# Kernel optimization log

Measured on AMD Instinct MI355X. Metric: run time of the kernel, lower is better.

The kernel has to match this reference:

```python
import jax, jax.numpy as jnp
import numpy as np

D_MODEL = 2048
N_EXPERTS = 64


def setup_inputs() -> dict:
    key = jax.random.key(0)
    kx, kw = jax.random.split(key)
    x = jax.random.normal(kx, (4, 4096, D_MODEL), dtype=jnp.float32)
    # nn.Linear(d_model, n_experts, bias=False): weight [n_experts, d_model]
    W = jax.random.normal(kw, (N_EXPERTS, D_MODEL), dtype=jnp.float32) * (1.0 / np.sqrt(D_MODEL))
    return {"x": x, "W": W, "n_active": 2, "capacity": 4096}


def reference(x, W, n_active, capacity):
    # router_logits = x @ W^T : [b, s, e]
    router_logits = jnp.einsum("bsd,ed->bse", x, W)
    router_probs = jax.nn.softmax(router_logits, axis=-1)
    # top-k over experts
    scores, expert_indices = jax.lax.top_k(router_probs, n_active)  # [b, s, k]
    scores = scores / jnp.sum(scores, axis=-1, keepdims=True)
    n_experts = router_probs.shape[-1]
    # scatter normalized scores into dense gate tensor [b, s, e]
    # (top-k indices are distinct, so one-hot sum == torch scatter_)
    gates = jnp.sum(
        jax.nn.one_hot(expert_indices, n_experts, dtype=scores.dtype) * scores[..., None],
        axis=-2,
    )
    expert_counts = jnp.sum(gates, axis=(0, 1))  # [e]
    load_loss = jnp.mean((expert_counts / jnp.sum(expert_counts) * n_experts - 1.0) ** 2)
    return gates, expert_indices, load_loss
```

## Files before the change

### kernel.cpp

```cpp
#include <hip/hip_runtime.h>
#include <hip/hip_bf16.h>
#include <math.h>

#define TOK_TOTAL 16384
#define D_MODEL   2048
#define NEXP      64
#define BM        32
#define KC        64
#define NCH       (D_MODEL / KC)
#define NBLK      (TOK_TOTAL / BM)
#define TAU       1e-3f

#define IDX_OFF   (TOK_TOTAL * NEXP)
#define LOSS_OFF  (IDX_OFF + TOK_TOTAL * 2)

#define WS_WL     65536
#define WS_CNTP   (2 * 65536)
#define WS_RCNT   (WS_CNTP + NBLK * NEXP)
#define WS_RLIST  (WS_RCNT + 1)

typedef __attribute__((ext_vector_type(8))) short short8_t;
typedef __attribute__((ext_vector_type(4))) float f32x4;

__device__ __forceinline__ short cvh(float f) {
    return __builtin_bit_cast(short, __float2bfloat16(f));
}
__device__ __forceinline__ short cvl(float f) {
    __hip_bfloat16 h = __float2bfloat16(f);
    return __builtin_bit_cast(short, __float2bfloat16(f - __bfloat162float(h)));
}

__device__ __forceinline__ void gload16(const void* gp, void* lp) {
    __builtin_amdgcn_global_load_lds(
        (const __attribute__((address_space(1))) void*)gp,
        (__attribute__((address_space(3))) void*)lp, 16, 0, 0);
}

__global__ __launch_bounds__(256, 1)
void build_wt(const float* __restrict__ W, short8_t* __restrict__ WH8,
              short8_t* __restrict__ WL8, int* __restrict__ rep_cnt)
{
    const int id = blockIdx.x * 256 + threadIdx.x;
    if (id == 0) *rep_cnt = 0;
    const int k8 = id & 255, e = id >> 8;
    float4 a = *(const float4*)(W + (long)e * D_MODEL + k8 * 8);
    float4 b = *(const float4*)(W + (long)e * D_MODEL + k8 * 8 + 4);
    short8_t h8, l8;
    h8[0]=cvh(a.x); h8[1]=cvh(a.y); h8[2]=cvh(a.z); h8[3]=cvh(a.w);
    h8[4]=cvh(b.x); h8[5]=cvh(b.y); h8[6]=cvh(b.z); h8[7]=cvh(b.w);
    l8[0]=cvl(a.x); l8[1]=cvl(a.y); l8[2]=cvl(a.z); l8[3]=cvl(a.w);
    l8[4]=cvl(b.x); l8[5]=cvl(b.y); l8[6]=cvl(b.z); l8[7]=cvl(b.w);
    WH8[k8 * NEXP + e] = h8;
    WL8[k8 * NEXP + e] = l8;
}

__global__ __launch_bounds__(256, 2)
void router_gemm(const float* __restrict__ x,
                 const short8_t* __restrict__ WH8, const short8_t* __restrict__ WL8,
                 float* __restrict__ out, float* __restrict__ cntp,
                 int* __restrict__ rep_cnt, int* __restrict__ rep_list)
{
    __shared__ __align__(16) float    sxf[2][BM][KC];
    __shared__ __align__(16) short8_t swh[2][8][NEXP];
    __shared__ __align__(16) short8_t swl[2][8][NEXP];
    __shared__ float4 s_ig[BM];

    const int t = threadIdx.x;
    const int w = t >> 6, l = t & 63;
    const int tg = w >> 1, eg = w & 1;
    const int lane16 = l & 15, kq = l >> 4;
    const long tok0 = (long)blockIdx.x * BM;
    const int arow = tg * 16 + lane16;

    f32x4 acc0 = (f32x4){0.f,0.f,0.f,0.f};
    f32x4 acc1 = (f32x4){0.f,0.f,0.f,0.f};

    auto STAGE = [&](int c, int buf) {
        #pragma unroll
        for (int j = 0; j < 2; ++j) {
            const int rbase = w * 8 + j * 4;
            const int r  = rbase + (l >> 4);
            const int s4 = (l & 15) ^ (r & 15);
            gload16(x + (tok0 + r) * D_MODEL + c * KC + s4 * 4, &sxf[buf][rbase][0]);
        }
        #pragma unroll
        for (int j = 0; j < 2; ++j) {
            const int k8 = w * 2 + j;
            gload16(WH8 + ((long)c * 8 + k8) * NEXP + l, &swh[buf][k8][0]);
            gload16(WL8 + ((long)c * 8 + k8) * NEXP + l, &swl[buf][k8][0]);
        }
    };

    auto COMPUTE = [&](int buf) {
        #pragma unroll
        for (int seg = 0; seg < 2; ++seg) {
            const int c4  = seg * 8 + kq * 2;
            f32x4 fa = *(const f32x4*)&sxf[buf][arow][((c4    ) ^ lane16) * 4];
            f32x4 fb = *(const f32x4*)&sxf[buf][arow][((c4 + 1) ^ lane16) * 4];
            short8_t ah, al;
            ah[0]=cvh(fa[0]); ah[1]=cvh(fa[1]); ah[2]=cvh(fa[2]); ah[3]=cvh(fa[3]);
            ah[4]=cvh(fb[0]); ah[5]=cvh(fb[1]); ah[6]=cvh(fb[2]); ah[7]=cvh(fb[3]);
            al[0]=cvl(fa[0]); al[1]=cvl(fa[1]); al[2]=cvl(fa[2]); al[3]=cvl(fa[3]);
            al[4]=cvl(fb[0]); al[5]=cvl(fb[1]); al[6]=cvl(fb[2]); al[7]=cvl(fb[3]);
            const int k8 = seg * 4 + kq;
            short8_t bh0 = swh[buf][k8][eg * 32 + lane16];
            short8_t bl0 = swl[buf][k8][eg * 32 + lane16];
            short8_t bh1 = swh[buf][k8][eg * 32 + 16 + lane16];
            short8_t bl1 = swl[buf][k8][eg * 32 + 16 + lane16];
            acc0 = __builtin_amdgcn_mfma_f32_16x16x32_bf16(ah, bl0, acc0, 0, 0, 0);
            acc0 = __builtin_amdgcn_mfma_f32_16x16x32_bf16(al, bh0, acc0, 0, 0, 0);
            acc0 = __builtin_amdgcn_mfma_f32_16x16x32_bf16(ah, bh0, acc0, 0, 0, 0);
            acc1 = __builtin_amdgcn_mfma_f32_16x16x32_bf16(ah, bl1, acc1, 0, 0, 0);
            acc1 = __builtin_amdgcn_mfma_f32_16x16x32_bf16(al, bh1, acc1, 0, 0, 0);
            acc1 = __builtin_amdgcn_mfma_f32_16x16x32_bf16(ah, bh1, acc1, 0, 0, 0);
        }
    };

    STAGE(0, 0);
    __syncthreads();

    for (int c = 0; c < NCH; ++c) {
        const int buf = c & 1;
        if (c + 1 < NCH) STAGE(c + 1, buf ^ 1);
        COMPUTE(buf);
        __syncthreads();
    }

    float* Lg = (float*)&sxf[0][0][0];
    {
        const int trow = tg * 16 + kq * 4;
        #pragma unroll
        for (int r = 0; r < 4; ++r) {
            Lg[(trow + r) * 68 + eg * 32 + lane16]      = acc0[r];
            Lg[(trow + r) * 68 + eg * 32 + 16 + lane16] = acc1[r];
        }
    }
    __syncthreads();

    if (t < BM) {
        const float* lrow = Lg + t * 68;
        float b0 = -1e30f, b1 = -1e30f, b2 = -1e30f;
        int i0 = 0, i1 = 0;
        for (int e = 0; e < NEXP; ++e) {
            float v = lrow[e];
            if (v > b0)      { b2 = b1; b1 = b0; i1 = i0; b0 = v; i0 = e; }
            else if (v > b1) { b2 = b1; b1 = v; i1 = e; }
            else if (v > b2) { b2 = v; }
        }
        float ex = __expf(b1 - b0);
        float g0 = 1.f / (1.f + ex);
        long tok = tok0 + t;
        out[IDX_OFF + 2 * tok]     = (float)i0;
        out[IDX_OFF + 2 * tok + 1] = (float)i1;
        s_ig[t] = make_float4((float)i0, (float)i1, g0, ex * g0);
        if ((b0 - b1 < TAU) || (b1 - b2 < TAU)) {
            int p = atomicAdd(rep_cnt, 1);
            rep_list[p] = (int)tok;
        }
    }
    __syncthreads();

    {
        const int r8 = t >> 3, e0 = (t & 7) * 8;
        float4 gg = s_ig[r8];
        const int i0 = (int)gg.x, i1 = (int)gg.y;
        float v[8];
        #pragma unroll
        for (int j = 0; j < 8; ++j) {
            int e = e0 + j;
            v[j] = (e == i0) ? gg.z : ((e == i1) ? gg.w : 0.f);
        }
        float* orow = out + (tok0 + r8) * NEXP + e0;
        *(float4*)(orow)     = make_float4(v[0], v[1], v[2], v[3]);
        *(float4*)(orow + 4) = make_float4(v[4], v[5], v[6], v[7]);
    }

    if (t < NEXP) {
        float cs = 0.f;
        for (int tt = 0; tt < BM; ++tt) {
            float4 gg = s_ig[tt];
            if ((int)gg.x == t) cs += gg.z;
            if ((int)gg.y == t) cs += gg.w;
        }
        cntp[blockIdx.x * NEXP + t] = cs;
    }
}

__global__ __launch_bounds__(256, 1)
void router_tail(const float* __restrict__ x, const float* __restrict__ W,
                 float* __restrict__ out, const float* __restrict__ cntp,
                 const int* __restrict__ rep_cnt, const int* __restrict__ rep_list)
{
    const int t = threadIdx.x;

    if (blockIdx.x == 0) {
        __shared__ double red[4][NEXP];
        const int e = t & 63, p = t >> 6;
        double s = 0.0;
        for (int b = 0; b < NBLK / 4; ++b)
            s += (double)cntp[(p * (NBLK / 4) + b) * NEXP + e];
        red[p][e] = s;
        __syncthreads();
        if (t == 0) {
            double sc[NEXP], tot = 0.0;
            for (int i = 0; i < NEXP; ++i) {
                sc[i] = red[0][i] + red[1][i] + red[2][i] + red[3][i];
                tot += sc[i];
            }
            double loss = 0.0;
            for (int i = 0; i < NEXP; ++i) {
                double d = sc[i] / tot * (double)NEXP - 1.0;
                loss += d * d;
            }
            out[LOSS_OFF] = (float)(loss / NEXP);
        }
        return;
    }

    __shared__ double red[4][NEXP];
    const int nf = *rep_cnt;
    const int e = t & 63, part = t >> 6;
    for (int i = (int)blockIdx.x - 1; i < nf; i += (int)gridDim.x - 1) {
        const long tok = rep_list[i];
        const float* xr = x + tok * D_MODEL;
        const float* wr = W + (long)e * D_MODEL;
        const int k0 = part * 512;
        double s = 0.0;
        for (int kk = 0; kk < 512; kk += 4) {
            float4 xv = *(const float4*)(xr + k0 + kk);
            float4 wv = *(const float4*)(wr + k0 + kk);
            s = fma((double)xv.x, (double)wv.x, s);
            s = fma((double)xv.y, (double)wv.y, s);
            s = fma((double)xv.z, (double)wv.z, s);
            s = fma((double)xv.w, (double)wv.w, s);
        }
        red[part][e] = s;
        __syncthreads();
        if (t == 0) {
            double best = -1e300, sec = -1e300;
            int bi = 0, si = 0;
            for (int ee = 0; ee < NEXP; ++ee) {
                double vv = red[0][ee] + red[1][ee] + red[2][ee] + red[3][ee];
                if (vv > best)     { sec = best; si = bi; best = vv; bi = ee; }
                else if (vv > sec) { sec = vv; si = ee; }
            }
            out[IDX_OFF + 2 * tok]     = (float)bi;
            out[IDX_OFF + 2 * tok + 1] = (float)si;
        }
        __syncthreads();
    }
}

extern "C" void kernel_launch(void* const* d_in, const int* in_sizes, int n_in,
                              void* d_out, int out_size, void* d_ws, size_t ws_size,
                              hipStream_t stream)
{
    const float* x = (const float*)d_in[0];
    const float* W = (const float*)d_in[1];
    float* out = (float*)d_out;
    float* ws  = (float*)d_ws;
    short8_t* WH8 = (short8_t*)ws;
    short8_t* WL8 = (short8_t*)(ws + WS_WL);
    float* cntp = ws + WS_CNTP;
    int* rep_cnt  = (int*)(ws + WS_RCNT);
    int* rep_list = (int*)(ws + WS_RLIST);

    build_wt   <<<64, 256, 0, stream>>>(W, WH8, WL8, rep_cnt);
    router_gemm<<<NBLK, 256, 0, stream>>>(x, WH8, WL8, out, cntp, rep_cnt, rep_list);
    router_tail<<<257, 256, 0, stream>>>(x, W, out, cntp, rep_cnt, rep_list);
}
```

Measured before the change: 89.61 us.

## Precompute bf16 hi/lo split of x in a separate pass before the GEMM

Adds a prep kernel that converts x from fp32 into separate bf16 high and low arrays in workspace. The router GEMM then stages these pre-split tiles into shared memory with an XOR swizzle, which removes the per-chunk conversion from the inner loop. The cost is an extra full read and two writes of the activation tensor, plus a third kernel launch. The shared-memory layout and the logits row stride are changed to match.

```diff
diff --git a/kernel.cpp b/kernel.cpp
--- a/kernel.cpp
+++ b/kernel.cpp
@@ -14,8 +14,12 @@
 #define IDX_OFF   (TOK_TOTAL * NEXP)
 #define LOSS_OFF  (IDX_OFF + TOK_TOTAL * 2)
 
-#define WS_WL     65536
-#define WS_CNTP   (2 * 65536)
+#define NX8       (TOK_TOTAL * 256)
+#define WS_XH     0
+#define WS_XL     (NX8 * 4)
+#define WS_WH     (2 * NX8 * 4)
+#define WS_WL     (WS_WH + 65536)
+#define WS_CNTP   (WS_WL + 65536)
 #define WS_RCNT   (WS_CNTP + NBLK * NEXP)
 #define WS_RLIST  (WS_RCNT + 1)
 
@@ -36,12 +40,33 @@
         (__attribute__((address_space(3))) void*)lp, 16, 0, 0);
 }
 
+__global__ __launch_bounds__(256, 8)
+void prep_x(const float* __restrict__ x, short8_t* __restrict__ XH8,
+            short8_t* __restrict__ XL8, int* __restrict__ rep_cnt)
+{
+    const int tid = blockIdx.x * 256 + threadIdx.x;
+    if (tid == 0) *rep_cnt = 0;
+    const f32x4* x4 = (const f32x4*)x;
+    #pragma unroll
+    for (int i = 0; i < 8; ++i) {
+        const long g8 = (long)tid + (long)i * (2048 * 256);
+        f32x4 a = __builtin_nontemporal_load(x4 + g8 * 2);
+        f32x4 b = __builtin_nontemporal_load(x4 + g8 * 2 + 1);
+        short8_t h8, l8;
+        h8[0]=cvh(a[0]); h8[1]=cvh(a[1]); h8[2]=cvh(a[2]); h8[3]=cvh(a[3]);
+        h8[4]=cvh(b[0]); h8[5]=cvh(b[1]); h8[6]=cvh(b[2]); h8[7]=cvh(b[3]);
+        l8[0]=cvl(a[0]); l8[1]=cvl(a[1]); l8[2]=cvl(a[2]); l8[3]=cvl(a[3]);
+        l8[4]=cvl(b[0]); l8[5]=cvl(b[1]); l8[6]=cvl(b[2]); l8[7]=cvl(b[3]);
+        XH8[g8] = h8;
+        XL8[g8] = l8;
+    }
+}
+
 __global__ __launch_bounds__(256, 1)
 void build_wt(const float* __restrict__ W, short8_t* __restrict__ WH8,
-              short8_t* __restrict__ WL8, int* __restrict__ rep_cnt)
+              short8_t* __restrict__ WL8)
 {
     const int id = blockIdx.x * 256 + threadIdx.x;
-    if (id == 0) *rep_cnt = 0;
     const int k8 = id & 255, e = id >> 8;
     float4 a = *(const float4*)(W + (long)e * D_MODEL + k8 * 8);
     float4 b = *(const float4*)(W + (long)e * D_MODEL + k8 * 8 + 4);
@@ -55,15 +80,17 @@
 }
 
 __global__ __launch_bounds__(256, 2)
-void router_gemm(const float* __restrict__ x,
+void router_gemm(const short8_t* __restrict__ XH8, const short8_t* __restrict__ XL8,
                  const short8_t* __restrict__ WH8, const short8_t* __restrict__ WL8,
                  float* __restrict__ out, float* __restrict__ cntp,
                  int* __restrict__ rep_cnt, int* __restrict__ rep_list)
 {
-    __shared__ __align__(16) float    sxf[2][BM][KC];
-    __shared__ __align__(16) short8_t swh[2][8][NEXP];
-    __shared__ __align__(16) short8_t swl[2][8][NEXP];
+    __shared__ __align__(16) short smem[24576];
     __shared__ float4 s_ig[BM];
+    short* sxh = smem;
+    short* sxl = smem + 4096;
+    short8_t* swh = (short8_t*)(smem + 8192);
+    short8_t* swl = (short8_t*)(smem + 16384);
 
     const int t = threadIdx.x;
     const int w = t >> 6, l = t & 63;
@@ -76,37 +103,32 @@
     f32x4 acc1 = (f32x4){0.f,0.f,0.f,0.f};
 
     auto STAGE = [&](int c, int buf) {
-        #pragma unroll
-        for (int j = 0; j < 2; ++j) {
-            const int rbase = w * 8 + j * 4;
-            const int r  = rbase + (l >> 4);
-            const int s4 = (l & 15) ^ (r & 15);
-            gload16(x + (tok0 + r) * D_MODEL + c * KC + s4 * 4, &sxf[buf][rbase][0]);
+        {
+            const int r  = w * 8 + (l >> 3);
+            const int s  = (l & 7) ^ (r & 7);
+            const long src = (tok0 + r) * 256 + c * 8 + s;
+            gload16(XH8 + src, sxh + (buf * 32 + w * 8) * 64);
+            gload16(XL8 + src, sxl + (buf * 32 + w * 8) * 64);
         }
         #pragma unroll
         for (int j = 0; j < 2; ++j) {
             const int k8 = w * 2 + j;
-            gload16(WH8 + ((long)c * 8 + k8) * NEXP + l, &swh[buf][k8][0]);
-            gload16(WL8 + ((long)c * 8 + k8) * NEXP + l, &swl[buf][k8][0]);
+            gload16(WH8 + ((long)c * 8 + k8) * NEXP + l, swh + (buf * 8 + k8) * NEXP);
+            gload16(WL8 + ((long)c * 8 + k8) * NEXP + l, swl + (buf * 8 + k8) * NEXP);
         }
     };
 
     auto COMPUTE = [&](int buf) {
         #pragma unroll
         for (int seg = 0; seg < 2; ++seg) {
-            const int c4  = seg * 8 + kq * 2;
-            f32x4 fa = *(const f32x4*)&sxf[buf][arow][((c4    ) ^ lane16) * 4];
-            f32x4 fb = *(const f32x4*)&sxf[buf][arow][((c4 + 1) ^ lane16) * 4];
-            short8_t ah, al;
-            ah[0]=cvh(fa[0]); ah[1]=cvh(fa[1]); ah[2]=cvh(fa[2]); ah[3]=cvh(fa[3]);
-            ah[4]=cvh(fb[0]); ah[5]=cvh(fb[1]); ah[6]=cvh(fb[2]); ah[7]=cvh(fb[3]);
-            al[0]=cvl(fa[0]); al[1]=cvl(fa[1]); al[2]=cvl(fa[2]); al[3]=cvl(fa[3]);
-            al[4]=cvl(fb[0]); al[5]=cvl(fb[1]); al[6]=cvl(fb[2]); al[7]=cvl(fb[3]);
+            const int slot = (seg * 4 + kq) ^ (arow & 7);
+            short8_t ah = *(const short8_t*)(sxh + (buf * 32 + arow) * 64 + slot * 8);
+            short8_t al = *(const short8_t*)(sxl + (buf * 32 + arow) * 64 + slot * 8);
             const int k8 = seg * 4 + kq;
-            short8_t bh0 = swh[buf][k8][eg * 32 + lane16];
-            short8_t bl0 = swl[buf][k8][eg * 32 + lane16];
-            short8_t bh1 = swh[buf][k8][eg * 32 + 16 + lane16];
-            short8_t bl1 = swl[buf][k8][eg * 32 + 16 + lane16];
+            short8_t bh0 = swh[(buf * 8 + k8) * NEXP + eg * 32 + lane16];
+            short8_t bl0 = swl[(buf * 8 + k8) * NEXP + eg * 32 + lane16];
+            short8_t bh1 = swh[(buf * 8 + k8) * NEXP + eg * 32 + 16 + lane16];
+            short8_t bl1 = swl[(buf * 8 + k8) * NEXP + eg * 32 + 16 + lane16];
             acc0 = __builtin_amdgcn_mfma_f32_16x16x32_bf16(ah, bl0, acc0, 0, 0, 0);
             acc0 = __builtin_amdgcn_mfma_f32_16x16x32_bf16(al, bh0, acc0, 0, 0, 0);
             acc0 = __builtin_amdgcn_mfma_f32_16x16x32_bf16(ah, bh0, acc0, 0, 0, 0);
@@ -126,19 +148,19 @@
         __syncthreads();
     }
 
-    float* Lg = (float*)&sxf[0][0][0];
+    float* Lg = (float*)smem;
     {
         const int trow = tg * 16 + kq * 4;
         #pragma unroll
         for (int r = 0; r < 4; ++r) {
-            Lg[(trow + r) * 68 + eg * 32 + lane16]      = acc0[r];
-            Lg[(trow + r) * 68 + eg * 32 + 16 + lane16] = acc1[r];
+            Lg[(trow + r) * 67 + eg * 32 + lane16]      = acc0[r];
+            Lg[(trow + r) * 67 + eg * 32 + 16 + lane16] = acc1[r];
         }
     }
     __syncthreads();
 
     if (t < BM) {
-        const float* lrow = Lg + t * 68;
+        const float* lrow = Lg + t * 67;
         float b0 = -1e30f, b1 = -1e30f, b2 = -1e30f;
         int i0 = 0, i1 = 0;
         for (int e = 0; e < NEXP; ++e) {
@@ -259,13 +281,16 @@
     const float* W = (const float*)d_in[1];
     float* out = (float*)d_out;
     float* ws  = (float*)d_ws;
-    short8_t* WH8 = (short8_t*)ws;
+    short8_t* XH8 = (short8_t*)(ws + WS_XH);
+    short8_t* XL8 = (short8_t*)(ws + WS_XL);
+    short8_t* WH8 = (short8_t*)(ws + WS_WH);
     short8_t* WL8 = (short8_t*)(ws + WS_WL);
     float* cntp = ws + WS_CNTP;
     int* rep_cnt  = (int*)(ws + WS_RCNT);
     int* rep_list = (int*)(ws + WS_RLIST);
 
-    build_wt   <<<64, 256, 0, stream>>>(W, WH8, WL8, rep_cnt);
-    router_gemm<<<NBLK, 256, 0, stream>>>(x, WH8, WL8, out, cntp, rep_cnt, rep_list);
+    prep_x     <<<2048, 256, 0, stream>>>(x, XH8, XL8, rep_cnt);
+    build_wt   <<<64, 256, 0, stream>>>(W, WH8, WL8);
+    router_gemm<<<NBLK, 256, 0, stream>>>(XH8, XL8, WH8, WL8, out, cntp, rep_cnt, rep_list);
     router_tail<<<257, 256, 0, stream>>>(x, W, out, cntp, rep_cnt, rep_list);
 }
```

After: 126.2 us. 40.8% more time.

## Stage full 16-token x tile in LDS and split K across waves

Applied to the files above, without the earlier changes.

The GEMM kernel now loads an entire 16x2048 fp32 x tile (128KB) into LDS in one shot instead of double-buffered 64-wide K chunks. 512 threads split the work so each wave owns one 16-expert slice and half of K, then the two halves are summed through LDS. W fragments are read directly from global memory (L2-resident) instead of being staged. This removes per-chunk barriers and gives more blocks, at the cost of one block per CU from the large LDS footprint and no overlap between load and compute within a block.

```diff
diff --git a/kernel.cpp b/kernel.cpp
--- a/kernel.cpp
+++ b/kernel.cpp
@@ -5,9 +5,7 @@
 #define TOK_TOTAL 16384
 #define D_MODEL   2048
 #define NEXP      64
-#define BM        32
-#define KC        64
-#define NCH       (D_MODEL / KC)
+#define BM        16
 #define NBLK      (TOK_TOTAL / BM)
 #define TAU       1e-3f
 
@@ -54,91 +52,70 @@
     WL8[k8 * NEXP + e] = l8;
 }
 
-__global__ __launch_bounds__(256, 2)
+__global__ __launch_bounds__(512, 1)
 void router_gemm(const float* __restrict__ x,
                  const short8_t* __restrict__ WH8, const short8_t* __restrict__ WL8,
                  float* __restrict__ out, float* __restrict__ cntp,
                  int* __restrict__ rep_cnt, int* __restrict__ rep_list)
 {
-    __shared__ __align__(16) float    sxf[2][BM][KC];
-    __shared__ __align__(16) short8_t swh[2][8][NEXP];
-    __shared__ __align__(16) short8_t swl[2][8][NEXP];
+    __shared__ __align__(16) float sx[BM][D_MODEL];
+    __shared__ float  Lg[BM][68];
     __shared__ float4 s_ig[BM];
 
     const int t = threadIdx.x;
     const int w = t >> 6, l = t & 63;
-    const int tg = w >> 1, eg = w & 1;
+    const int g = w & 3, h = w >> 2;
     const int lane16 = l & 15, kq = l >> 4;
     const long tok0 = (long)blockIdx.x * BM;
-    const int arow = tg * 16 + lane16;
-
-    f32x4 acc0 = (f32x4){0.f,0.f,0.f,0.f};
-    f32x4 acc1 = (f32x4){0.f,0.f,0.f,0.f};
-
-    auto STAGE = [&](int c, int buf) {
-        #pragma unroll
-        for (int j = 0; j < 2; ++j) {
-            const int rbase = w * 8 + j * 4;
-            const int r  = rbase + (l >> 4);
-            const int s4 = (l & 15) ^ (r & 15);
-            gload16(x + (tok0 + r) * D_MODEL + c * KC + s4 * 4, &sxf[buf][rbase][0]);
-        }
-        #pragma unroll
-        for (int j = 0; j < 2; ++j) {
-            const int k8 = w * 2 + j;
-            gload16(WH8 + ((long)c * 8 + k8) * NEXP + l, &swh[buf][k8][0]);
-            gload16(WL8 + ((long)c * 8 + k8) * NEXP + l, &swl[buf][k8][0]);
-        }
-    };
-
-    auto COMPUTE = [&](int buf) {
-        #pragma unroll
-        for (int seg = 0; seg < 2; ++seg) {
-            const int c4  = seg * 8 + kq * 2;
-            f32x4 fa = *(const f32x4*)&sxf[buf][arow][((c4    ) ^ lane16) * 4];
-            f32x4 fb = *(const f32x4*)&sxf[buf][arow][((c4 + 1) ^ lane16) * 4];
-            short8_t ah, al;
-            ah[0]=cvh(fa[0]); ah[1]=cvh(fa[1]); ah[2]=cvh(fa[2]); ah[3]=cvh(fa[3]);
-            ah[4]=cvh(fb[0]); ah[5]=cvh(fb[1]); ah[6]=cvh(fb[2]); ah[7]=cvh(fb[3]);
-            al[0]=cvl(fa[0]); al[1]=cvl(fa[1]); al[2]=cvl(fa[2]); al[3]=cvl(fa[3]);
-            al[4]=cvl(fb[0]); al[5]=cvl(fb[1]); al[6]=cvl(fb[2]); al[7]=cvl(fb[3]);
-            const int k8 = seg * 4 + kq;
-            short8_t bh0 = swh[buf][k8][eg * 32 + lane16];
-            short8_t bl0 = swl[buf][k8][eg * 32 + lane16];
-            short8_t bh1 = swh[buf][k8][eg * 32 + 16 + lane16];
-            short8_t bl1 = swl[buf][k8][eg * 32 + 16 + lane16];
-            acc0 = __builtin_amdgcn_mfma_f32_16x16x32_bf16(ah, bl0, acc0, 0, 0, 0);
-            acc0 = __builtin_amdgcn_mfma_f32_16x16x32_bf16(al, bh0, acc0, 0, 0, 0);
-            acc0 = __builtin_amdgcn_mfma_f32_16x16x32_bf16(ah, bh0, acc0, 0, 0, 0);
-            acc1 = __builtin_amdgcn_mfma_f32_16x16x32_bf16(ah, bl1, acc1, 0, 0, 0);
-            acc1 = __builtin_amdgcn_mfma_f32_16x16x32_bf16(al, bh1, acc1, 0, 0, 0);
-            acc1 = __builtin_amdgcn_mfma_f32_16x16x32_bf16(ah, bh1, acc1, 0, 0, 0);
-        }
-    };
-
-    STAGE(0, 0);
-    __syncthreads();
-
-    for (int c = 0; c < NCH; ++c) {
-        const int buf = c & 1;
-        if (c + 1 < NCH) STAGE(c + 1, buf ^ 1);
-        COMPUTE(buf);
-        __syncthreads();
-    }
-
-    float* Lg = (float*)&sxf[0][0][0];
+
     {
-        const int trow = tg * 16 + kq * 4;
-        #pragma unroll
-        for (int r = 0; r < 4; ++r) {
-            Lg[(trow + r) * 68 + eg * 32 + lane16]      = acc0[r];
-            Lg[(trow + r) * 68 + eg * 32 + 16 + lane16] = acc1[r];
-        }
+        const float4* xs = (const float4*)x + tok0 * (D_MODEL / 4);
+        float4* sx4 = (float4*)&sx[0][0];
+        #pragma unroll
+        for (int i = 0; i < 16; ++i) {
+            const int base = i * 512 + w * 64;
+            gload16(xs + base + l, sx4 + base);
+        }
+    }
+    __syncthreads();
+
+    f32x4 acc = (f32x4){0.f, 0.f, 0.f, 0.f};
+    const short8_t* WHp = WH8 + g * 16 + lane16;
+    const short8_t* WLp = WL8 + g * 16 + lane16;
+    const int ks0 = h * 32;
+    #pragma unroll 4
+    for (int ks = ks0; ks < ks0 + 32; ++ks) {
+        const int kk = ks * 32 + kq * 8;
+        f32x4 fa = *(const f32x4*)&sx[lane16][kk];
+        f32x4 fb = *(const f32x4*)&sx[lane16][kk + 4];
+        short8_t ah, al;
+        ah[0]=cvh(fa[0]); ah[1]=cvh(fa[1]); ah[2]=cvh(fa[2]); ah[3]=cvh(fa[3]);
+        ah[4]=cvh(fb[0]); ah[5]=cvh(fb[1]); ah[6]=cvh(fb[2]); ah[7]=cvh(fb[3]);
+        al[0]=cvl(fa[0]); al[1]=cvl(fa[1]); al[2]=cvl(fa[2]); al[3]=cvl(fa[3]);
+        al[4]=cvl(fb[0]); al[5]=cvl(fb[1]); al[6]=cvl(fb[2]); al[7]=cvl(fb[3]);
+        const long k8 = (long)(ks * 4 + kq) * NEXP;
+        short8_t bh = WHp[k8];
+        short8_t bl = WLp[k8];
+        acc = __builtin_amdgcn_mfma_f32_16x16x32_bf16(ah, bl, acc, 0, 0, 0);
+        acc = __builtin_amdgcn_mfma_f32_16x16x32_bf16(al, bh, acc, 0, 0, 0);
+        acc = __builtin_amdgcn_mfma_f32_16x16x32_bf16(ah, bh, acc, 0, 0, 0);
+    }
+
+    if (h == 0) {
+        #pragma unroll
+        for (int r = 0; r < 4; ++r)
+            Lg[kq * 4 + r][g * 16 + lane16] = acc[r];
+    }
+    __syncthreads();
+    if (h == 1) {
+        #pragma unroll
+        for (int r = 0; r < 4; ++r)
+            Lg[kq * 4 + r][g * 16 + lane16] += acc[r];
     }
     __syncthreads();
 
     if (t < BM) {
-        const float* lrow = Lg + t * 68;
+        const float* lrow = Lg[t];
         float b0 = -1e30f, b1 = -1e30f, b2 = -1e30f;
         int i0 = 0, i1 = 0;
         for (int e = 0; e < NEXP; ++e) {
@@ -160,19 +137,17 @@
     }
     __syncthreads();
 
-    {
-        const int r8 = t >> 3, e0 = (t & 7) * 8;
-        float4 gg = s_ig[r8];
+    if (t < 256) {
+        const int r = t >> 4, e0 = (t & 15) * 4;
+        float4 gg = s_ig[r];
         const int i0 = (int)gg.x, i1 = (int)gg.y;
-        float v[8];
-        #pragma unroll
-        for (int j = 0; j < 8; ++j) {
+        float v[4];
+        #pragma unroll
+        for (int j = 0; j < 4; ++j) {
             int e = e0 + j;
             v[j] = (e == i0) ? gg.z : ((e == i1) ? gg.w : 0.f);
         }
-        float* orow = out + (tok0 + r8) * NEXP + e0;
-        *(float4*)(orow)     = make_float4(v[0], v[1], v[2], v[3]);
-        *(float4*)(orow + 4) = make_float4(v[4], v[5], v[6], v[7]);
+        *(float4*)(out + (tok0 + r) * NEXP + e0) = make_float4(v[0], v[1], v[2], v[3]);
     }
 
     if (t < NEXP) {
@@ -266,6 +241,6 @@
     int* rep_list = (int*)(ws + WS_RLIST);
 
     build_wt   <<<64, 256, 0, stream>>>(W, WH8, WL8, rep_cnt);
-    router_gemm<<<NBLK, 256, 0, stream>>>(x, WH8, WL8, out, cntp, rep_cnt, rep_list);
+    router_gemm<<<NBLK, 512, 0, stream>>>(x, WH8, WL8, out, cntp, rep_cnt, rep_list);
     router_tail<<<257, 256, 0, stream>>>(x, W, out, cntp, rep_cnt, rep_list);
 }
```

Measured after the change: 122.2 us. +36.4%, slower.
